# Kernel optimization log

Measured on AMD Instinct MI355X. Metric: run time of the kernel, lower is better.

The kernel has to match this reference:

```python
import jax, jax.numpy as jnp
import numpy as np

N_IN = 200000   # active input voxels
N_OUT = 200000  # active output voxels (stride-1 conv)
K = 27          # kernel volume = 3^3 hypercube, dimension=3
M = 150000      # kernel-map pairs per offset
C_IN = 64
C_OUT = 64


def setup_inputs() -> dict:
    key = jax.random.key(0)
    k1, k2, k3, k4 = jax.random.split(key, 4)
    in_feats = jax.random.normal(k1, (N_IN, C_IN), dtype=jnp.float32)
    kernel = jax.random.normal(k2, (K, C_IN, C_OUT), dtype=jnp.float32) * (1.0 / np.sqrt(C_IN * K))
    in_map = jax.random.randint(k3, (K, M), 0, N_IN, dtype=jnp.int32)
    out_map = jax.random.randint(k4, (K, M), 0, N_OUT, dtype=jnp.int32)
    return {"in_feats": in_feats, "kernel": kernel, "in_map": in_map, "out_map": out_map}


def reference(in_feats, kernel, in_map, out_map):
    """Sparse conv: per kernel offset k, gather input rows via in_map[k],
    GEMM with kernel[k], scatter-add into output rows via out_map[k].
    Scan over the K=27 offsets keeps peak memory at one [M, C_OUT] buffer."""
    c_out = kernel.shape[-1]

    def step(out, offset):
        w_k, im_k, om_k = offset          # [C_IN,C_OUT], [M], [M]
        gathered = in_feats[im_k]         # [M, C_IN] gather
        contrib = gathered @ w_k          # [M, C_OUT] per-offset GEMM
        out = out.at[om_k].add(contrib)   # scatter-add
        return out, None

    out0 = jnp.zeros((N_OUT, c_out), dtype=in_feats.dtype)
    out, _ = jax.lax.scan(step, out0, (kernel, in_map, out_map))
    return out
```

## Files before the change

kernel.cpp:

```cpp
#include <hip/hip_runtime.h>
#include <hip/hip_bf16.h>
#include <stdint.h>

#define KVOL   27
#define MPAIRS 150000
#define NROWS  200000
#define CDIM   64
#define TOTALC (KVOL*MPAIRS)

#define NPASS  3
#define KPP    9
#define PASSC  (KPP*MPAIRS)
#define BROWS  128
#define NBKT   1563
#define NPB    (NPASS*NBKT)
#define SUBW   8
#define NWGH   (KVOL*SUBW)
#define CHUNKH (MPAIRS/SUBW)
#define CELLS  (NPB*NWGH)
#define ECAP   1280

typedef __attribute__((ext_vector_type(8))) short bf16x8;
typedef __attribute__((ext_vector_type(4))) float f32x4;
typedef __attribute__((ext_vector_type(2))) unsigned long long u64x2;

__device__ __forceinline__ unsigned short f2bfu(float f) {
  union { float f; uint32_t u; } v; v.f = f;
  uint32_t u = v.u;
  u += 0x7FFF + ((u >> 16) & 1);
  return (unsigned short)(u >> 16);
}
__device__ __forceinline__ short f2bf(float f) { return (short)f2bfu(f); }
__device__ __forceinline__ float bf2f(uint32_t u16) {
  union { uint32_t u; float f; } v; v.u = u16 << 16; return v.f;
}

__global__ void cvt_all(const float* __restrict__ in, short* __restrict__ out,
                        const float* __restrict__ w, short* __restrict__ wt, int n8) {
  if (blockIdx.x < KVOL) {
    int k = blockIdx.x;
    const float* wk = w + (size_t)k * CDIM * CDIM;
    short* wtk = wt + (size_t)k * CDIM * CDIM;
    for (int t = threadIdx.x; t < CDIM * CDIM; t += blockDim.x) {
      int j = t >> 6, i = t & 63;
      wtk[j * CDIM + i] = f2bf(wk[i * CDIM + j]);
    }
    return;
  }
  int i = (blockIdx.x - KVOL) * blockDim.x + threadIdx.x;
  int stride = (gridDim.x - KVOL) * blockDim.x;
  for (; i < n8; i += stride) {
    const float* p = in + (size_t)i * 8;
    f32x4 f0 = *(const f32x4*)(p);
    f32x4 f1 = *(const f32x4*)(p + 4);
    bf16x8 o;
    o[0] = f2bf(f0[0]); o[1] = f2bf(f0[1]); o[2] = f2bf(f0[2]); o[3] = f2bf(f0[3]);
    o[4] = f2bf(f1[0]); o[5] = f2bf(f1[1]); o[6] = f2bf(f1[2]); o[7] = f2bf(f1[3]);
    *(bf16x8*)(out + (size_t)i * 8) = o;
  }
}

__global__ __launch_bounds__(256)
void k_hist(const int* __restrict__ om, unsigned int* __restrict__ hist_g) {
  __shared__ unsigned int h[NBKT];
  const int wg = blockIdx.x, tid = threadIdx.x;
  const int k = wg / SUBW, sub = wg - k * SUBW;
  const int pass = k / KPP;
  for (int i = tid; i < NBKT; i += 256) h[i] = 0u;
  __syncthreads();
  const int base = k * MPAIRS + sub * CHUNKH;
  for (int i = tid; i < CHUNKH; i += 256)
    atomicAdd(&h[((unsigned)om[base + i]) >> 7], 1u);
  __syncthreads();
  for (int b = tid; b < NBKT; b += 256)
    hist_g[(size_t)(pass * NBKT + b) * NWGH + wg] = h[b];
}

__global__ void scan_local(const unsigned int* __restrict__ counts,
                           unsigned int* __restrict__ offsets,
                           unsigned int* __restrict__ bsum, int n) {
  __shared__ unsigned int sh[1024];
  int t = threadIdx.x;
  int idx = blockIdx.x * 1024 + t;
  unsigned int v = (idx < n) ? counts[idx] : 0u;
  sh[t] = v; __syncthreads();
  for (int o = 1; o < 1024; o <<= 1) {
    unsigned int u = (t >= o) ? sh[t - o] : 0u;
    __syncthreads();
    sh[t] += u;
    __syncthreads();
  }
  if (idx < n) offsets[idx] = sh[t] - v;
  if (t == 1023) bsum[blockIdx.x] = sh[1023];
}

__global__ void scan_bsum(unsigned int* __restrict__ bsum, int nb) {
  __shared__ unsigned int sh[1024];
  int t = threadIdx.x;
  unsigned int v = (t < nb) ? bsum[t] : 0u;
  sh[t] = v; __syncthreads();
  for (int o = 1; o < 1024; o <<= 1) {
    unsigned int u = (t >= o) ? sh[t - o] : 0u;
    __syncthreads();
    sh[t] += u;
    __syncthreads();
  }
  if (t < nb) bsum[t] = sh[t] - v;
}

__global__ void scan_apply(unsigned int* __restrict__ offsets,
                           const unsigned int* __restrict__ bsum,
                           const unsigned int* __restrict__ counts, int n) {
  int idx = blockIdx.x * 1024 + threadIdx.x;
  if (idx < n) {
    unsigned int o = offsets[idx] + bsum[blockIdx.x];
    offsets[idx] = o;
    if (idx == n - 1) offsets[n] = o + counts[idx];
  }
}

__global__ __launch_bounds__(256)
void k_scatter(const int* __restrict__ om,
               const unsigned int* __restrict__ offs, unsigned int* __restrict__ sorted_g) {
  __shared__ unsigned int cur[NBKT];
  const int wg = blockIdx.x, tid = threadIdx.x;
  const int k = wg / SUBW, sub = wg - k * SUBW;
  const int pass = k / KPP, kk = k - pass * KPP;
  for (int b = tid; b < NBKT; b += 256)
    cur[b] = offs[(size_t)(pass * NBKT + b) * NWGH + wg];
  __syncthreads();
  const int base = k * MPAIRS + sub * CHUNKH;
  const unsigned int elb = (unsigned)(kk * MPAIRS + sub * CHUNKH);
  for (int i = tid; i < CHUNKH; i += 256) {
    unsigned int o = (unsigned)om[base + i];
    unsigned int pos = atomicAdd(&cur[o >> 7], 1u);
    sorted_g[pos] = ((o & 127u) << 21) | (elb + (unsigned)i);
  }
}

__global__ __launch_bounds__(256, 8)
void k_gemm(const short* __restrict__ a_bf16, const short* __restrict__ wt_bf16,
            const int* __restrict__ in_map, short* __restrict__ contrib, int pass)
{
  const int kk   = blockIdx.y;
  const int k    = pass * KPP + kk;
  const int lane = threadIdx.x & 63;
  const int wave = threadIdx.x >> 6;
  const int r    = lane & 15;
  const int h    = lane >> 4;

  bf16x8 b[4][2];
  const short* wtk = wt_bf16 + (size_t)k * CDIM * CDIM;
#pragma unroll
  for (int t = 0; t < 4; ++t)
#pragma unroll
    for (int c = 0; c < 2; ++c)
      b[t][c] = *(const bf16x8*)(wtk + (t * 16 + r) * CDIM + c * 32 + h * 8);

  const int* imk = in_map + (size_t)k * MPAIRS;
  const int ntiles = MPAIRS / 16;
  const int wstride = gridDim.x * 4;

  const int p0 = h & 1, p1 = h >> 1;

  for (int tile = blockIdx.x * 4 + wave; tile < ntiles; tile += wstride) {
    const int base = tile * 16;
    const int in_row = imk[base + r];
    const short* arow = a_bf16 + (size_t)in_row * CDIM;
    bf16x8 a0 = *(const bf16x8*)(arow + h * 8);
    bf16x8 a1 = *(const bf16x8*)(arow + 32 + h * 8);

    f32x4 acc[4];
#pragma unroll
    for (int t = 0; t < 4; ++t) {
      acc[t] = (f32x4){0.f, 0.f, 0.f, 0.f};
      acc[t] = __builtin_amdgcn_mfma_f32_16x16x32_bf16(b[t][0], a0, acc[t], 0, 0, 0);
      acc[t] = __builtin_amdgcn_mfma_f32_16x16x32_bf16(b[t][1], a1, acc[t], 0, 0, 0);
    }

    unsigned long long pk0, pk1, pk2, pk3;
    {
      unsigned long long p_[4];
#pragma unroll
      for (int t = 0; t < 4; ++t)
        p_[t] = (unsigned long long)f2bfu(acc[t][0])
              | ((unsigned long long)f2bfu(acc[t][1]) << 16)
              | ((unsigned long long)f2bfu(acc[t][2]) << 32)
              | ((unsigned long long)f2bfu(acc[t][3]) << 48);
      pk0 = p_[0]; pk1 = p_[1]; pk2 = p_[2]; pk3 = p_[3];
    }
    {
      unsigned long long s1 = p0 ? pk0 : pk1;
      s1 = __shfl_xor(s1, 16);
      if (p0) pk0 = s1; else pk1 = s1;
      unsigned long long s3 = p0 ? pk2 : pk3;
      s3 = __shfl_xor(s3, 16);
      if (p0) pk2 = s3; else pk3 = s3;
    }
    short* crow = contrib + (size_t)(kk * MPAIRS + base + r) * CDIM;
    u64x2 A; A[0] = pk0; A[1] = pk1;
    u64x2 B; B[0] = pk2; B[1] = pk3;
    __builtin_nontemporal_store(A, (u64x2*)(crow + p0 * 16 + p1 * 8));
    __builtin_nontemporal_store(B, (u64x2*)(crow + 32 + p0 * 16 + p1 * 8));
  }
}

__global__ __launch_bounds__(512, 4)
void k_reduce(const short* __restrict__ contrib,
              const unsigned int* __restrict__ sorted_g,
              const unsigned int* __restrict__ offs,
              float* __restrict__ out, int pass)
{
  __shared__ unsigned int ents[ECAP];
  __shared__ unsigned int h[BROWS], bs[BROWS], cur[BROWS];

  const int bkt = blockIdx.x, tid = threadIdx.x;
  const int bin = pass * NBKT + bkt;
  const unsigned int s = offs[(size_t)bin * NWGH];
  const unsigned int e = offs[(size_t)(bin + 1) * NWGH];
  int cnt = (int)(e - s); if (cnt > ECAP) cnt = ECAP;

  if (tid < BROWS) h[tid] = 0u;
  __syncthreads();
  for (int i = tid; i < cnt; i += 512)
    atomicAdd(&h[sorted_g[s + i] >> 21], 1u);
  __syncthreads();
  if (tid < BROWS) bs[tid] = h[tid];
  __syncthreads();
#pragma unroll
  for (int o = 1; o < BROWS; o <<= 1) {
    unsigned int v = 0;
    if (tid < BROWS && tid >= o) v = bs[tid - o];
    __syncthreads();
    if (tid < BROWS) bs[tid] += v;
    __syncthreads();
  }
  if (tid < BROWS) {
    unsigned int ex = bs[tid] - h[tid];
    bs[tid] = ex;
    cur[tid] = ex;
  }
  __syncthreads();
  for (int i = tid; i < cnt; i += 512) {
    unsigned int en = sorted_g[s + i];
    unsigned int pos = atomicAdd(&cur[en >> 21], 1u);
    ents[pos] = en;
  }
  __syncthreads();

  const int lane = tid & 63, wv = tid >> 6;
  const int q    = lane >> 4;
  const int cl4  = lane & 15;
  const unsigned long long* cb = (const unsigned long long*)contrib;

#pragma unroll 1
  for (int rp = 0; rp < 4; ++rp) {
    const int row  = wv * 16 + rp * 4 + q;
    const int grow = bkt * BROWS + row;
    const bool active = (grow < NROWS) && !(h[row] == 0u && pass);
    if (active) {
      float a0 = 0.f, a1 = 0.f, a2 = 0.f, a3 = 0.f;
      float b0 = 0.f, b1 = 0.f, b2 = 0.f, b3 = 0.f;
      int j = (int)bs[row];
      const int je = j + (int)h[row];
      for (; j + 3 < je; j += 4) {
        unsigned long long w0 = __builtin_nontemporal_load(&cb[(size_t)(ents[j]     & 0x1FFFFFu) * 16 + cl4]);
        unsigned long long w1 = __builtin_nontemporal_load(&cb[(size_t)(ents[j + 1] & 0x1FFFFFu) * 16 + cl4]);
        unsigned long long w2 = __builtin_nontemporal_load(&cb[(size_t)(ents[j + 2] & 0x1FFFFFu) * 16 + cl4]);
        unsigned long long w3 = __builtin_nontemporal_load(&cb[(size_t)(ents[j + 3] & 0x1FFFFFu) * 16 + cl4]);
        a0 += bf2f((uint32_t)w0 & 0xFFFFu); a1 += bf2f(((uint32_t)w0) >> 16);
        a2 += bf2f((uint32_t)(w0 >> 32) & 0xFFFFu); a3 += bf2f((uint32_t)(w0 >> 48));
        b0 += bf2f((uint32_t)w1 & 0xFFFFu); b1 += bf2f(((uint32_t)w1) >> 16);
        b2 += bf2f((uint32_t)(w1 >> 32) & 0xFFFFu); b3 += bf2f((uint32_t)(w1 >> 48));
        a0 += bf2f((uint32_t)w2 & 0xFFFFu); a1 += bf2f(((uint32_t)w2) >> 16);
        a2 += bf2f((uint32_t)(w2 >> 32) & 0xFFFFu); a3 += bf2f((uint32_t)(w2 >> 48));
        b0 += bf2f((uint32_t)w3 & 0xFFFFu); b1 += bf2f(((uint32_t)w3) >> 16);
        b2 += bf2f((uint32_t)(w3 >> 32) & 0xFFFFu); b3 += bf2f((uint32_t)(w3 >> 48));
      }
      if (j + 1 < je) {
        unsigned long long w0 = __builtin_nontemporal_load(&cb[(size_t)(ents[j]     & 0x1FFFFFu) * 16 + cl4]);
        unsigned long long w1 = __builtin_nontemporal_load(&cb[(size_t)(ents[j + 1] & 0x1FFFFFu) * 16 + cl4]);
        a0 += bf2f((uint32_t)w0 & 0xFFFFu); a1 += bf2f(((uint32_t)w0) >> 16);
        a2 += bf2f((uint32_t)(w0 >> 32) & 0xFFFFu); a3 += bf2f((uint32_t)(w0 >> 48));
        b0 += bf2f((uint32_t)w1 & 0xFFFFu); b1 += bf2f(((uint32_t)w1) >> 16);
        b2 += bf2f((uint32_t)(w1 >> 32) & 0xFFFFu); b3 += bf2f((uint32_t)(w1 >> 48));
        j += 2;
      }
      if (j < je) {
        unsigned long long w0 = __builtin_nontemporal_load(&cb[(size_t)(ents[j] & 0x1FFFFFu) * 16 + cl4]);
        a0 += bf2f((uint32_t)w0 & 0xFFFFu); a1 += bf2f(((uint32_t)w0) >> 16);
        a2 += bf2f((uint32_t)(w0 >> 32) & 0xFFFFu); a3 += bf2f((uint32_t)(w0 >> 48));
      }
      a0 += b0; a1 += b1; a2 += b2; a3 += b3;
      float* op = out + (size_t)grow * CDIM + cl4 * 4;
      if (pass) {
        float4 prev = *(const float4*)op;
        a0 += prev.x; a1 += prev.y; a2 += prev.z; a3 += prev.w;
      }
      float4 o4; o4.x = a0; o4.y = a1; o4.z = a2; o4.w = a3;
      *(float4*)op = o4;
    }
  }
}

extern "C" void kernel_launch(void* const* d_in, const int* in_sizes, int n_in,
                              void* d_out, int out_size, void* d_ws, size_t ws_size,
                              hipStream_t stream) {
  const float* in_feats = (const float*)d_in[0];
  const float* kernel   = (const float*)d_in[1];
  const int*   in_map   = (const int*)d_in[2];
  const int*   out_map  = (const int*)d_in[3];
  float* out = (float*)d_out;

  uint8_t* ws = (uint8_t*)d_ws;
  size_t off = 0;
  auto alloc = [&](size_t bytes) -> void* {
    void* p = ws + off;
    off += (bytes + 255) & ~(size_t)255;
    return p;
  };
  short* in_bf16         = (short*)alloc((size_t)NROWS * CDIM * 2);
  short* wt_bf16         = (short*)alloc((size_t)KVOL * CDIM * CDIM * 2);
  unsigned int* hist_g   = (unsigned int*)alloc((size_t)CELLS * 4);
  unsigned int* offs     = (unsigned int*)alloc((size_t)(CELLS + 1) * 4);
  unsigned int* bsum     = (unsigned int*)alloc(4096);
  unsigned int* sorted_g = (unsigned int*)alloc((size_t)TOTALC * 4);
  short* contrib         = (short*)alloc((size_t)PASSC * CDIM * 2);

  hipMemsetAsync(hist_g, 0, (size_t)CELLS * 4, stream);

  cvt_all<<<2048 + KVOL, 256, 0, stream>>>(in_feats, in_bf16, kernel, wt_bf16,
                                           NROWS * CDIM / 8);

  k_hist<<<NWGH, 256, 0, stream>>>(out_map, hist_g);

  const int sb = (CELLS + 1023) / 1024;
  scan_local<<<sb, 1024, 0, stream>>>(hist_g, offs, bsum, CELLS);
  scan_bsum<<<1, 1024, 0, stream>>>(bsum, sb);
  scan_apply<<<sb, 1024, 0, stream>>>(offs, bsum, hist_g, CELLS);

  k_scatter<<<NWGH, 256, 0, stream>>>(out_map, offs, sorted_g);

  for (int p = 0; p < NPASS; ++p) {
    dim3 g(227, KPP);
    k_gemm<<<g, 256, 0, stream>>>(in_bf16, wt_bf16, in_map, contrib, p);
    k_reduce<<<NBKT, 512, 0, stream>>>(contrib, sorted_g, offs, out, p);
  }
}
```

Measured before the change: 441.5 us.

## Use a single pass over all kernel offsets when workspace is large enough

The number of passes becomes a runtime choice based on workspace size: with enough workspace, all 27 offsets go into one bf16 contrib buffer and get one GEMM and one reduce launch instead of three of each. The packed entry index widens by one bit and the per-bucket entry capacity grows to cover the larger bucket populations. This removes the repeated read-modify-write of the output and two sets of launches and tails, at the cost of a much larger contrib buffer and more shared memory in the reduce kernel, which may lower its occupancy. If the workspace is smaller, it falls back to three passes.

```diff
diff --git a/kernel.cpp b/kernel.cpp
--- a/kernel.cpp
+++ b/kernel.cpp
@@ -8,17 +8,12 @@
 #define CDIM   64
 #define TOTALC (KVOL*MPAIRS)
 
-#define NPASS  3
-#define KPP    9
-#define PASSC  (KPP*MPAIRS)
 #define BROWS  128
 #define NBKT   1563
-#define NPB    (NPASS*NBKT)
 #define SUBW   8
 #define NWGH   (KVOL*SUBW)
 #define CHUNKH (MPAIRS/SUBW)
-#define CELLS  (NPB*NWGH)
-#define ECAP   1280
+#define ECAP   3072
 
 typedef __attribute__((ext_vector_type(8))) short bf16x8;
 typedef __attribute__((ext_vector_type(4))) float f32x4;
@@ -61,11 +56,11 @@
 }
 
 __global__ __launch_bounds__(256)
-void k_hist(const int* __restrict__ om, unsigned int* __restrict__ hist_g) {
+void k_hist(const int* __restrict__ om, unsigned int* __restrict__ hist_g, int kpp) {
   __shared__ unsigned int h[NBKT];
   const int wg = blockIdx.x, tid = threadIdx.x;
   const int k = wg / SUBW, sub = wg - k * SUBW;
-  const int pass = k / KPP;
+  const int pass = k / kpp;
   for (int i = tid; i < NBKT; i += 256) h[i] = 0u;
   __syncthreads();
   const int base = k * MPAIRS + sub * CHUNKH;
@@ -121,11 +116,12 @@
 
 __global__ __launch_bounds__(256)
 void k_scatter(const int* __restrict__ om,
-               const unsigned int* __restrict__ offs, unsigned int* __restrict__ sorted_g) {
+               const unsigned int* __restrict__ offs, unsigned int* __restrict__ sorted_g,
+               int kpp) {
   __shared__ unsigned int cur[NBKT];
   const int wg = blockIdx.x, tid = threadIdx.x;
   const int k = wg / SUBW, sub = wg - k * SUBW;
-  const int pass = k / KPP, kk = k - pass * KPP;
+  const int pass = k / kpp, kk = k - pass * kpp;
   for (int b = tid; b < NBKT; b += 256)
     cur[b] = offs[(size_t)(pass * NBKT + b) * NWGH + wg];
   __syncthreads();
@@ -134,16 +130,17 @@
   for (int i = tid; i < CHUNKH; i += 256) {
     unsigned int o = (unsigned)om[base + i];
     unsigned int pos = atomicAdd(&cur[o >> 7], 1u);
-    sorted_g[pos] = ((o & 127u) << 21) | (elb + (unsigned)i);
+    sorted_g[pos] = ((o & 127u) << 22) | (elb + (unsigned)i);
   }
 }
 
 __global__ __launch_bounds__(256, 8)
 void k_gemm(const short* __restrict__ a_bf16, const short* __restrict__ wt_bf16,
-            const int* __restrict__ in_map, short* __restrict__ contrib, int pass)
+            const int* __restrict__ in_map, short* __restrict__ contrib,
+            int pass, int kpp)
 {
   const int kk   = blockIdx.y;
-  const int k    = pass * KPP + kk;
+  const int k    = pass * kpp + kk;
   const int lane = threadIdx.x & 63;
   const int wave = threadIdx.x >> 6;
   const int r    = lane & 15;
@@ -223,7 +220,7 @@
   if (tid < BROWS) h[tid] = 0u;
   __syncthreads();
   for (int i = tid; i < cnt; i += 512)
-    atomicAdd(&h[sorted_g[s + i] >> 21], 1u);
+    atomicAdd(&h[sorted_g[s + i] >> 22], 1u);
   __syncthreads();
   if (tid < BROWS) bs[tid] = h[tid];
   __syncthreads();
@@ -243,7 +240,7 @@
   __syncthreads();
   for (int i = tid; i < cnt; i += 512) {
     unsigned int en = sorted_g[s + i];
-    unsigned int pos = atomicAdd(&cur[en >> 21], 1u);
+    unsigned int pos = atomicAdd(&cur[en >> 22], 1u);
     ents[pos] = en;
   }
   __syncthreads();
@@ -264,10 +261,10 @@
       int j = (int)bs[row];
       const int je = j + (int)h[row];
       for (; j + 3 < je; j += 4) {
-        unsigned long long w0 = __builtin_nontemporal_load(&cb[(size_t)(ents[j]     & 0x1FFFFFu) * 16 + cl4]);
-        unsigned long long w1 = __builtin_nontemporal_load(&cb[(size_t)(ents[j + 1] & 0x1FFFFFu) * 16 + cl4]);
-        unsigned long long w2 = __builtin_nontemporal_load(&cb[(size_t)(ents[j + 2] & 0x1FFFFFu) * 16 + cl4]);
-        unsigned long long w3 = __builtin_nontemporal_load(&cb[(size_t)(ents[j + 3] & 0x1FFFFFu) * 16 + cl4]);
+        unsigned long long w0 = __builtin_nontemporal_load(&cb[(size_t)(ents[j]     & 0x3FFFFFu) * 16 + cl4]);
+        unsigned long long w1 = __builtin_nontemporal_load(&cb[(size_t)(ents[j + 1] & 0x3FFFFFu) * 16 + cl4]);
+        unsigned long long w2 = __builtin_nontemporal_load(&cb[(size_t)(ents[j + 2] & 0x3FFFFFu) * 16 + cl4]);
+        unsigned long long w3 = __builtin_nontemporal_load(&cb[(size_t)(ents[j + 3] & 0x3FFFFFu) * 16 + cl4]);
         a0 += bf2f((uint32_t)w0 & 0xFFFFu); a1 += bf2f(((uint32_t)w0) >> 16);
         a2 += bf2f((uint32_t)(w0 >> 32) & 0xFFFFu); a3 += bf2f((uint32_t)(w0 >> 48));
         b0 += bf2f((uint32_t)w1 & 0xFFFFu); b1 += bf2f(((uint32_t)w1) >> 16);
@@ -278,8 +275,8 @@
         b2 += bf2f((uint32_t)(w3 >> 32) & 0xFFFFu); b3 += bf2f((uint32_t)(w3 >> 48));
       }
       if (j + 1 < je) {
-        unsigned long long w0 = __builtin_nontemporal_load(&cb[(size_t)(ents[j]     & 0x1FFFFFu) * 16 + cl4]);
-        unsigned long long w1 = __builtin_nontemporal_load(&cb[(size_t)(ents[j + 1] & 0x1FFFFFu) * 16 + cl4]);
+        unsigned long long w0 = __builtin_nontemporal_load(&cb[(size_t)(ents[j]     & 0x3FFFFFu) * 16 + cl4]);
+        unsigned long long w1 = __builtin_nontemporal_load(&cb[(size_t)(ents[j + 1] & 0x3FFFFFu) * 16 + cl4]);
         a0 += bf2f((uint32_t)w0 & 0xFFFFu); a1 += bf2f(((uint32_t)w0) >> 16);
         a2 += bf2f((uint32_t)(w0 >> 32) & 0xFFFFu); a3 += bf2f((uint32_t)(w0 >> 48));
         b0 += bf2f((uint32_t)w1 & 0xFFFFu); b1 += bf2f(((uint32_t)w1) >> 16);
@@ -287,7 +284,7 @@
         j += 2;
       }
       if (j < je) {
-        unsigned long long w0 = __builtin_nontemporal_load(&cb[(size_t)(ents[j] & 0x1FFFFFu) * 16 + cl4]);
+        unsigned long long w0 = __builtin_nontemporal_load(&cb[(size_t)(ents[j] & 0x3FFFFFu) * 16 + cl4]);
         a0 += bf2f((uint32_t)w0 & 0xFFFFu); a1 += bf2f(((uint32_t)w0) >> 16);
         a2 += bf2f((uint32_t)(w0 >> 32) & 0xFFFFu); a3 += bf2f((uint32_t)(w0 >> 48));
       }
@@ -312,6 +309,11 @@
   const int*   out_map  = (const int*)d_in[3];
   float* out = (float*)d_out;
 
+  const int npass = (ws_size >= (size_t)575 * 1000 * 1000) ? 1 : 3;
+  const int kpp = KVOL / npass;
+  const int cells = npass * NBKT * NWGH;
+  const size_t passc = (size_t)kpp * MPAIRS;
+
   uint8_t* ws = (uint8_t*)d_ws;
   size_t off = 0;
   auto alloc = [&](size_t bytes) -> void* {
@@ -321,29 +323,29 @@
   };
   short* in_bf16         = (short*)alloc((size_t)NROWS * CDIM * 2);
   short* wt_bf16         = (short*)alloc((size_t)KVOL * CDIM * CDIM * 2);
-  unsigned int* hist_g   = (unsigned int*)alloc((size_t)CELLS * 4);
-  unsigned int* offs     = (unsigned int*)alloc((size_t)(CELLS + 1) * 4);
+  unsigned int* hist_g   = (unsigned int*)alloc((size_t)cells * 4);
+  unsigned int* offs     = (unsigned int*)alloc((size_t)(cells + 1) * 4);
   unsigned int* bsum     = (unsigned int*)alloc(4096);
   unsigned int* sorted_g = (unsigned int*)alloc((size_t)TOTALC * 4);
-  short* contrib         = (short*)alloc((size_t)PASSC * CDIM * 2);
-
-  hipMemsetAsync(hist_g, 0, (size_t)CELLS * 4, stream);
+  short* contrib         = (short*)alloc(passc * CDIM * 2);
+
+  hipMemsetAsync(hist_g, 0, (size_t)cells * 4, stream);
 
   cvt_all<<<2048 + KVOL, 256, 0, stream>>>(in_feats, in_bf16, kernel, wt_bf16,
                                            NROWS * CDIM / 8);
 
-  k_hist<<<NWGH, 256, 0, stream>>>(out_map, hist_g);
-
-  const int sb = (CELLS + 1023) / 1024;
-  scan_local<<<sb, 1024, 0, stream>>>(hist_g, offs, bsum, CELLS);
+  k_hist<<<NWGH, 256, 0, stream>>>(out_map, hist_g, kpp);
+
+  const int sb = (cells + 1023) / 1024;
+  scan_local<<<sb, 1024, 0, stream>>>(hist_g, offs, bsum, cells);
   scan_bsum<<<1, 1024, 0, stream>>>(bsum, sb);
-  scan_apply<<<sb, 1024, 0, stream>>>(offs, bsum, hist_g, CELLS);
-
-  k_scatter<<<NWGH, 256, 0, stream>>>(out_map, offs, sorted_g);
-
-  for (int p = 0; p < NPASS; ++p) {
-    dim3 g(227, KPP);
-    k_gemm<<<g, 256, 0, stream>>>(in_bf16, wt_bf16, in_map, contrib, p);
+  scan_apply<<<sb, 1024, 0, stream>>>(offs, bsum, hist_g, cells);
+
+  k_scatter<<<NWGH, 256, 0, stream>>>(out_map, offs, sorted_g, kpp);
+
+  for (int p = 0; p < npass; ++p) {
+    dim3 g(227, kpp);
+    k_gemm<<<g, 256, 0, stream>>>(in_bf16, wt_bf16, in_map, contrib, p, kpp);
     k_reduce<<<NBKT, 512, 0, stream>>>(contrib, sorted_g, offs, out, p);
   }
 }
```

Result: no change. 442.5 us (+0.2%).
